# Performance work log

Hardware: AMD Instinct MI355X
Metric: run time of the kernel (lower is better)

## Reference

```python
import jax, jax.numpy as jnp
import numpy as np

HEADS = 4
REDUCTION = 4
BN_EPS = 1e-5


def conv1x1_bn(x, W, b, gamma, beta, mean, var):
    # x: [B, C, W, H]; 1x1 conv == channel matmul, then BN (inference form)
    y = jnp.einsum('oc,bcwh->bowh', W, x) + b[None, :, None, None]
    scale = (gamma / jnp.sqrt(var + BN_EPS))[None, :, None, None]
    return (y - mean[None, :, None, None]) * scale + beta[None, :, None, None]


def setup_inputs() -> dict:
    key = jax.random.key(0)
    ks = jax.random.split(key, 24)
    C, Cq = 512, 512 // REDUCTION  # 128
    B, Wd, Hd = 16, 32, 32
    dh = Cq // HEADS  # 32
    rnd = lambda k, s: jax.random.normal(k, s, dtype=jnp.float32)
    pos = lambda k, s: jax.random.uniform(k, s, dtype=jnp.float32, minval=0.5, maxval=1.5)
    return {
        'x': rnd(ks[0], (B, C, Wd, Hd)),
        'Wq': rnd(ks[1], (Cq, C)) * 0.05, 'bq': rnd(ks[2], (Cq,)) * 0.05,
        'q_gamma': pos(ks[3], (Cq,)), 'q_beta': rnd(ks[4], (Cq,)) * 0.05,
        'q_mean': rnd(ks[5], (Cq,)) * 0.05, 'q_var': pos(ks[6], (Cq,)),
        'Wk': rnd(ks[7], (Cq, C)) * 0.05, 'bk': rnd(ks[8], (Cq,)) * 0.05,
        'k_gamma': pos(ks[9], (Cq,)), 'k_beta': rnd(ks[10], (Cq,)) * 0.05,
        'k_mean': rnd(ks[11], (Cq,)) * 0.05, 'k_var': pos(ks[12], (Cq,)),
        'Wv': rnd(ks[13], (C, C)) * 0.05, 'bv': rnd(ks[14], (C,)) * 0.05,
        'v_gamma': pos(ks[15], (C,)), 'v_beta': rnd(ks[16], (C,)) * 0.05,
        'v_mean': rnd(ks[17], (C,)) * 0.05, 'v_var': pos(ks[18], (C,)),
        'rel_h': rnd(ks[19], (1, HEADS, dh, 1, Hd)),
        'rel_w': rnd(ks[20], (1, HEADS, dh, Wd, 1)),
    }


def reference(x, Wq, bq, q_gamma, q_beta, q_mean, q_var,
              Wk, bk, k_gamma, k_beta, k_mean, k_var,
              Wv, bv, v_gamma, v_beta, v_mean, v_var,
              rel_h, rel_w):
    B, C, Wd, Hd = x.shape
    N = Wd * Hd
    dh = C // REDUCTION // HEADS
    dv = C // HEADS
    q = conv1x1_bn(x, Wq, bq, q_gamma, q_beta, q_mean, q_var).reshape(B, HEADS, dh, N)
    k = conv1x1_bn(x, Wk, bk, k_gamma, k_beta, k_mean, k_var).reshape(B, HEADS, dh, N)
    v = conv1x1_bn(x, Wv, bv, v_gamma, v_beta, v_mean, v_var).reshape(B, HEADS, dv, N)
    # content-content: q^T k -> [B, H, N, N]
    cc = jnp.einsum('bhdn,bhdm->bhnm', q, k)
    # content-position: (rel_h + rel_w) flattened to [H, dh, N], then pos^T @ q
    pos = (rel_h + rel_w).reshape(HEADS, dh, N)
    cp = jnp.einsum('hdn,bhdm->bhnm', pos, q)
    attn = jax.nn.softmax(cc + cp, axis=-1)
    # out = v @ attn^T  (torch: matmul(v, attention.permute(0,1,3,2)))
    out = jnp.einsum('bhcn,bhmn->bhcm', v, attn)
    return out.reshape(B, C, Wd, Hd) + x
```

## Files before the change

kernel.cpp:

```cpp
#include <hip/hip_runtime.h>


typedef _Float16 f16x8 __attribute__((ext_vector_type(8)));
typedef __attribute__((ext_vector_type(4))) float f32x4;
typedef __attribute__((ext_vector_type(4))) unsigned int u32x4;
typedef __attribute__((ext_vector_type(2))) unsigned int u32x2;

#define MFMAH(a, b, c) __builtin_amdgcn_mfma_f32_16x16x32_f16(a, b, c, 0, 0, 0)
#define LOG2E 1.4426950408889634f

__device__ __forceinline__ unsigned pkh(float a, float b) {
  auto p = __builtin_amdgcn_cvt_pkrtz(a, b);
  return __builtin_bit_cast(unsigned, p);
}
__device__ __forceinline__ short f2h(float a) {
  _Float16 h = (_Float16)a;
  return __builtin_bit_cast(short, h);
}

__device__ __forceinline__ void gload16(const void* g, void* l) {
  __builtin_amdgcn_global_load_lds(
      (const __attribute__((address_space(1))) void*)g,
      (__attribute__((address_space(3))) void*)l, 16, 0, 0);
}

__global__ __launch_bounds__(256) void fold_kernel(
    const float* __restrict__ Wq, const float* __restrict__ bq,
    const float* __restrict__ qg, const float* __restrict__ qbe,
    const float* __restrict__ qme, const float* __restrict__ qva,
    const float* __restrict__ Wk, const float* __restrict__ bk,
    const float* __restrict__ kg, const float* __restrict__ kbe,
    const float* __restrict__ kme, const float* __restrict__ kva,
    const float* __restrict__ Wv, const float* __restrict__ bv,
    const float* __restrict__ vg, const float* __restrict__ vbe,
    const float* __restrict__ vme, const float* __restrict__ vva,
    unsigned short* __restrict__ Wh, float* __restrict__ bfv)
{
  int idx = blockIdx.x * 256 + threadIdx.x;
  if (idx >= 768 * 512) return;
  int o = idx >> 9, c = idx & 511;
  float w, sc, bb, mean, beta, post;
  if (o < 128) {
    sc = qg[o] / sqrtf(qva[o] + 1e-5f);
    w = Wq[o * 512 + c]; bb = bq[o]; mean = qme[o]; beta = qbe[o];
    post = LOG2E;
  } else if (o < 256) {
    int r = o - 128;
    sc = kg[r] / sqrtf(kva[r] + 1e-5f);
    w = Wk[r * 512 + c]; bb = bk[r]; mean = kme[r]; beta = kbe[r];
    post = 1.0f;
  } else {
    int r = o - 256;
    sc = vg[r] / sqrtf(vva[r] + 1e-5f);
    w = Wv[r * 512 + c]; bb = bv[r]; mean = vme[r]; beta = vbe[r];
    post = 1.0f;
  }
  Wh[idx] = (unsigned short)f2h(w * sc * post);
  if (c == 0) bfv[o] = ((bb - mean) * sc + beta) * post;
}

__global__ __launch_bounds__(256) void pos_kernel(
    const float* __restrict__ rel_h, const float* __restrict__ rel_w,
    unsigned short* __restrict__ posH)
{
  int idx = blockIdx.x * 256 + threadIdx.x;
  if (idx >= 4 * 1024 * 32) return;
  int h = idx >> 15, rem = idx & 32767, n = rem >> 5, d = rem & 31;
  int w = n >> 5, hh = n & 31;
  float v = rel_h[(h * 32 + d) * 32 + hh] + rel_w[(h * 32 + d) * 32 + w];
  posH[idx] = (unsigned short)f2h(v);
}

__global__ __launch_bounds__(256) void proj_kernel(
    const float* __restrict__ x,
    const unsigned short* __restrict__ Wh, const float* __restrict__ bfv,
    unsigned short* __restrict__ qH, unsigned short* __restrict__ kH,
    unsigned short* __restrict__ vH)
{
  __shared__ __align__(16) short sm[16384];
  short* At = sm;
  short* Bt = sm + 8192;

  int bid = blockIdx.x;
  int b = bid / 48, rem = bid % 48, mblk = rem >> 3, nblk = rem & 7;
  int Mb = mblk * 128, Nb = nblk * 128;
  int t = threadIdx.x;
  int lane = t & 63, wvid = t >> 6, ln = lane & 15, g = lane >> 4;
  int wm = wvid >> 1, wn = wvid & 1;
  int kgp = t >> 5, lp = t & 31;

  f32x4 acc[4][4];
  for (int i = 0; i < 4; i++)
    for (int j = 0; j < 4; j++) acc[i][j] = (f32x4){0.f, 0.f, 0.f, 0.f};

  for (int kb = 0; kb < 512; kb += 64) {
    __syncthreads();
    for (int ii = 0; ii < 4; ii++) {
      int idx = ii * 256 + t;
      int row = idx >> 3, pos = idx & 7;
      int j = pos ^ (row & 7);
      *(f16x8*)&At[row * 64 + pos * 8] =
          *(const f16x8*)&Wh[(Mb + row) * 512 + kb + j * 8];
    }
    for (int e = 0; e < 2; e++) {
      float2 f[8];
      for (int rr = 0; rr < 8; rr++)
        f[rr] = *(const float2*)&x[(b * 512 + kb + kgp * 8 + rr) * 1024 +
                                   Nb + 2 * lp + 64 * e];
      int n0 = 2 * lp + 64 * e, n1 = n0 + 1;
      u32x4 h0, h1;
      for (int pr = 0; pr < 4; pr++) {
        h0[pr] = pkh(f[2 * pr].x, f[2 * pr + 1].x);
        h1[pr] = pkh(f[2 * pr].y, f[2 * pr + 1].y);
      }
      *(u32x4*)&Bt[n0 * 64 + 8 * (kgp ^ (n0 & 7))] = h0;
      *(u32x4*)&Bt[n1 * 64 + 8 * (kgp ^ (n1 & 7))] = h1;
    }
    __syncthreads();

    f16x8 af[4][2], bf[4][2];
    for (int mt = 0; mt < 4; mt++)
      for (int ks = 0; ks < 2; ks++) {
        int o = wm * 64 + mt * 16 + ln;
        af[mt][ks] = *(const f16x8*)&At[o * 64 + 8 * ((ks * 4 + g) ^ (o & 7))];
      }
    for (int nt = 0; nt < 4; nt++)
      for (int ks = 0; ks < 2; ks++) {
        int n = wn * 64 + nt * 16 + ln;
        bf[nt][ks] = *(const f16x8*)&Bt[n * 64 + 8 * ((ks * 4 + g) ^ (n & 7))];
      }
    for (int ks = 0; ks < 2; ks++)
      for (int mt = 0; mt < 4; mt++)
        for (int nt = 0; nt < 4; nt++)
          acc[mt][nt] = MFMAH(af[mt][ks], bf[nt][ks], acc[mt][nt]);
  }

  unsigned* smU = (unsigned*)sm;
  for (int p = 0; p < 2; p++) {
    __syncthreads();
    if (wn == p) {
      if (mblk < 2) {
        for (int mt = 0; mt < 4; mt++)
          for (int nt = 0; nt < 4; nt++) {
            float y0 = acc[mt][nt][0] + bfv[Mb + wm * 64 + mt * 16 + g * 4 + 0];
            float y1 = acc[mt][nt][1] + bfv[Mb + wm * 64 + mt * 16 + g * 4 + 1];
            float y2 = acc[mt][nt][2] + bfv[Mb + wm * 64 + mt * 16 + g * 4 + 2];
            float y3 = acc[mt][nt][3] + bfv[Mb + wm * 64 + mt * 16 + g * 4 + 3];
            u32x2 pk = (u32x2){pkh(y0, y1), pkh(y2, y3)};
            int nl = nt * 16 + ln;
            *(u32x2*)&smU[nl * 66 + wm * 32 + mt * 8 + g * 2] = pk;
          }
      } else {
        for (int mt = 0; mt < 4; mt++)
          for (int nt = 0; nt < 4; nt++)
            for (int r = 0; r < 4; r++) {
              int o = wm * 64 + mt * 16 + g * 4 + r;
              sm[o * 72 + nt * 16 + ln] = f2h(acc[mt][nt][r] + bfv[Mb + o]);
            }
      }
    }
    __syncthreads();
    if (mblk < 2) {
      unsigned short* dh = (mblk == 0) ? qH : kH;
      for (int it = 0; it < 4; it++) {
        int task = it * 256 + t;
        int h = task >> 8, nl = (task >> 2) & 63, qc = task & 3;
        u32x4 v4 = *(const u32x4*)&smU[nl * 66 + h * 16 + qc * 4];
        int gi = ((b * 4 + h) * 1024 + Nb + p * 64 + nl) * 32 + qc * 8;
        *(u32x4*)&dh[gi] = v4;
      }
    } else {
      int bh = b * 4 + (mblk - 2);
      for (int it = 0; it < 4; it++) {
        int task = it * 256 + t;
        int o = task >> 3, qc = task & 7;
        u32x4 vv = *(const u32x4*)&sm[o * 72 + qc * 8];
        *(u32x4*)&vH[(bh * 128 + o) * 1024 + Nb + p * 64 + qc * 8] = vv;
      }
    }
  }
}

__global__ __launch_bounds__(512, 4) void attn_kernel(
    const float* __restrict__ x,
    const unsigned short* __restrict__ qH, const unsigned short* __restrict__ kH,
    const unsigned short* __restrict__ posH, const unsigned short* __restrict__ vH,
    float* __restrict__ out)
{
  __shared__ __align__(16) short sm[2 * 12288 + 8 * 1152];

  int bid = blockIdx.x;
  int bh = (bid & 7) * 8 + ((bid >> 3) & 7);
  int qt = bid >> 6;
  int b = bh >> 2, h = bh & 3;
  int t = threadIdx.x;
  int lane = t & 63, w = t >> 6, ln = lane & 15, g = (lane >> 4) & 3;

  int qrow = qt * 128 + w * 16 + ln;
  f16x8 bQ   = *(const f16x8*)&qH[(bh * 1024 + qrow) * 32 + g * 8];
  f16x8 bPos = *(const f16x8*)&posH[(h * 1024 + qrow) * 32 + g * 8];

  f16x8 aOnes;
  {
    _Float16 o1 = (ln == 0) ? (_Float16)1.0f : (_Float16)0.0f;
    for (int i = 0; i < 8; i++) aOnes[i] = o1;
  }

  f32x4 acc[9];
  for (int ct = 0; ct < 9; ct++) acc[ct] = (f32x4){0.f, 0.f, 0.f, 0.f};
  float m_run = -1e30f;

  short* Pw = &sm[24576 + w * 1152];

  auto STAGE = [&](int bb, int jb) {
    {
      int u = t & 255;
      int r = u >> 2;
      int ch = (u & 3) ^ (r & 3) ^ ((r >> 2) & 3);
      long gq = (long)(bh * 1024 + jb + r) * 32 + ch * 8;
      const unsigned short* src = (t < 256) ? kH : qH;
      short* base = &sm[bb * 12288 + ((t < 256) ? 0 : 2048) + (w & 3) * 512];
      gload16(&src[gq], base);
    }
    for (int i = 0; i < 2; i++) {
      int u = t + i * 512;
      int c = u >> 3;
      int vch = (u & 7) ^ (c & 7);
      long gv = (long)(bh * 128 + c) * 1024 + jb + vch * 8;
      short* base = &sm[bb * 12288 + 4096 + (w + i * 8) * 512];
      gload16(&vH[gv], base);
    }
  };

  STAGE(0, 0);

  for (int it = 0; it < 16; ++it) {
    int cur = it & 1;
    if (it < 15) {
      STAGE(cur ^ 1, (it + 1) * 64);
      asm volatile("s_waitcnt vmcnt(3)" ::: "memory");
    } else {
      asm volatile("s_waitcnt vmcnt(0)" ::: "memory");
    }
    __builtin_amdgcn_s_barrier();
    __builtin_amdgcn_sched_barrier(0);

    const short* B = &sm[cur * 12288];

    f16x8 aK[4], aQ[4];
    for (int kt = 0; kt < 4; kt++) {
      int r = kt * 16 + ln;
      int p = g ^ (r & 3) ^ ((r >> 2) & 3);
      int off = r * 32 + p * 8;
      aK[kt] = *(const f16x8*)&B[off];
      aQ[kt] = *(const f16x8*)&B[2048 + off];
    }

    f32x4 s[4];
    for (int kt = 0; kt < 4; kt++) s[kt] = (f32x4){0.f, 0.f, 0.f, 0.f};
    __builtin_amdgcn_s_setprio(1);
    for (int kt = 0; kt < 4; kt++) s[kt] = MFMAH(aK[kt], bQ, s[kt]);
    for (int kt = 0; kt < 4; kt++) s[kt] = MFMAH(aQ[kt], bPos, s[kt]);
    __builtin_amdgcn_s_setprio(0);

    float m0 = fmaxf(fmaxf(s[0][0], s[0][1]), fmaxf(s[0][2], s[0][3]));
    float m1 = fmaxf(fmaxf(s[1][0], s[1][1]), fmaxf(s[1][2], s[1][3]));
    float m2 = fmaxf(fmaxf(s[2][0], s[2][1]), fmaxf(s[2][2], s[2][3]));
    float m3 = fmaxf(fmaxf(s[3][0], s[3][1]), fmaxf(s[3][2], s[3][3]));
    float mx = fmaxf(fmaxf(m0, m1), fmaxf(m2, m3));
    if (__any(mx > m_run + 8.f)) {
      float mxf = fmaxf(mx, __shfl_xor(mx, 16));
      mxf = fmaxf(mxf, __shfl_xor(mxf, 32));
      float mnew = fmaxf(m_run, mxf);
      float scl = __builtin_amdgcn_exp2f(m_run - mnew);
      for (int ct = 0; ct < 9; ct++) acc[ct] *= scl;
      m_run = mnew;
    }
    for (int kt = 0; kt < 4; kt++)
      for (int r = 0; r < 4; r++)
        s[kt][r] = __builtin_amdgcn_exp2f(s[kt][r] - m_run);

    for (int kt = 0; kt < 4; kt++) {
      u32x2 pk = (u32x2){pkh(s[kt][0], s[kt][1]), pkh(s[kt][2], s[kt][3])};
      *(u32x2*)&Pw[ln * 72 + kt * 16 + g * 4] = pk;
    }
    asm volatile("s_waitcnt lgkmcnt(0)" ::: "memory");
    __builtin_amdgcn_sched_barrier(0);
    f16x8 pFrag[2];
    for (int st2 = 0; st2 < 2; st2++)
      pFrag[st2] = *(const f16x8*)&Pw[ln * 72 + st2 * 32 + g * 8];

    __builtin_amdgcn_s_setprio(1);
    for (int ct = 0; ct < 8; ct++)
      for (int st2 = 0; st2 < 2; st2++) {
        int c = ct * 16 + ln;
        int pos = (st2 * 4 + g) ^ (c & 7);
        f16x8 av = *(const f16x8*)&B[4096 + c * 64 + pos * 8];
        acc[ct] = MFMAH(av, pFrag[st2], acc[ct]);
      }
    acc[8] = MFMAH(aOnes, pFrag[0], acc[8]);
    acc[8] = MFMAH(aOnes, pFrag[1], acc[8]);
    __builtin_amdgcn_s_setprio(0);

    __builtin_amdgcn_sched_barrier(0);
    __builtin_amdgcn_s_barrier();
    __builtin_amdgcn_sched_barrier(0);
  }

  float lsum = __shfl(acc[8][0], ln);
  float inv = 1.0f / lsum;
  int m = qt * 128 + w * 16 + ln;
  for (int ct = 0; ct < 8; ct++)
    for (int r = 0; r < 4; r++) {
      int c = h * 128 + ct * 16 + g * 4 + r;
      int gi = (b * 512 + c) * 1024 + m;
      out[gi] = acc[ct][r] * inv + x[gi];
    }
}

extern "C" void kernel_launch(void* const* d_in, const int* in_sizes, int n_in,
                              void* d_out, int out_size, void* d_ws, size_t ws_size,
                              hipStream_t stream) {
  const float* x    = (const float*)d_in[0];
  const float* Wq   = (const float*)d_in[1];
  const float* bq   = (const float*)d_in[2];
  const float* qg   = (const float*)d_in[3];
  const float* qbe  = (const float*)d_in[4];
  const float* qme  = (const float*)d_in[5];
  const float* qva  = (const float*)d_in[6];
  const float* Wk   = (const float*)d_in[7];
  const float* bk   = (const float*)d_in[8];
  const float* kg   = (const float*)d_in[9];
  const float* kbe  = (const float*)d_in[10];
  const float* kme  = (const float*)d_in[11];
  const float* kva  = (const float*)d_in[12];
  const float* Wv   = (const float*)d_in[13];
  const float* bv   = (const float*)d_in[14];
  const float* vg   = (const float*)d_in[15];
  const float* vbe  = (const float*)d_in[16];
  const float* vme  = (const float*)d_in[17];
  const float* vva  = (const float*)d_in[18];
  const float* relh = (const float*)d_in[19];
  const float* relw = (const float*)d_in[20];
  float* outp = (float*)d_out;

  unsigned char* ws = (unsigned char*)d_ws;
  unsigned short* Whp  = (unsigned short*)(ws + 0);
  float*          bfv  = (float*)(ws + 786432);
  unsigned short* qHp  = (unsigned short*)(ws + 789504);
  unsigned short* kHp  = (unsigned short*)(ws + 4983808);
  unsigned short* posHp= (unsigned short*)(ws + 9178112);
  unsigned short* vHp  = (unsigned short*)(ws + 9440256);

  fold_kernel<<<1536, 256, 0, stream>>>(Wq, bq, qg, qbe, qme, qva,
                                        Wk, bk, kg, kbe, kme, kva,
                                        Wv, bv, vg, vbe, vme, vva,
                                        Whp, bfv);
  pos_kernel<<<512, 256, 0, stream>>>(relh, relw, posHp);
  proj_kernel<<<768, 256, 0, stream>>>(x, Whp, bfv, qHp, kHp, vHp);
  attn_kernel<<<512, 512, 0, stream>>>(x, qHp, kHp, posHp, vHp, outp);
}
```

Before: 87.59 us.

## Double-buffer projection GEMM with async weight loads and register-prefetched x tiles

Restructures the projection GEMM main loop into a double-buffered software pipeline over 32-wide K steps. Weight tiles are fetched straight into LDS with global_load_lds, and the x tile for the next step is held in registers and written to LDS after the current MFMAs. This overlaps global loads with compute and removes one barrier per iteration. In exchange it uses a smaller K step (16 iterations instead of 8), a new XOR swizzle, and an s_setprio boost around the MFMAs. The extra register pressure may cost occupancy.

```diff
diff --git a/kernel.cpp b/kernel.cpp
--- a/kernel.cpp
+++ b/kernel.cpp
@@ -17,6 +17,7 @@
   _Float16 h = (_Float16)a;
   return __builtin_bit_cast(short, h);
 }
+__device__ __forceinline__ int sfn(int x) { return (x & 3) ^ ((x >> 2) & 3); }
 
 __device__ __forceinline__ void gload16(const void* g, void* l) {
   __builtin_amdgcn_global_load_lds(
@@ -78,66 +79,85 @@
     unsigned short* __restrict__ vH)
 {
   __shared__ __align__(16) short sm[16384];
-  short* At = sm;
-  short* Bt = sm + 8192;
 
   int bid = blockIdx.x;
   int b = bid / 48, rem = bid % 48, mblk = rem >> 3, nblk = rem & 7;
   int Mb = mblk * 128, Nb = nblk * 128;
   int t = threadIdx.x;
-  int lane = t & 63, wvid = t >> 6, ln = lane & 15, g = lane >> 4;
-  int wm = wvid >> 1, wn = wvid & 1;
+  int lane = t & 63, w4 = t >> 6, ln = lane & 15, g = lane >> 4;
+  int wm = w4 >> 1, wn = w4 & 1;
   int kgp = t >> 5, lp = t & 31;
+  int n0b = 2 * lp, hh = kgp & 1, cch = kgp >> 1;
 
   f32x4 acc[4][4];
   for (int i = 0; i < 4; i++)
     for (int j = 0; j < 4; j++) acc[i][j] = (f32x4){0.f, 0.f, 0.f, 0.f};
 
-  for (int kb = 0; kb < 512; kb += 64) {
+  float2 fB[8];
+
+  auto ISSUE_B = [&](int kb) {
+    for (int e = 0; e < 2; e++)
+      for (int rr = 0; rr < 4; rr++)
+        fB[e * 4 + rr] = *(const float2*)&x[(b * 512 + kb + kgp * 4 + rr) * 1024 +
+                                            Nb + n0b + e * 64];
+  };
+  auto ISSUE_A = [&](int kb, int bb) {
+    for (int i = 0; i < 2; i++) {
+      int grp = w4 + i * 4;
+      int unit = grp * 64 + lane;
+      int row = unit >> 2, pos = unit & 3;
+      int j = pos ^ sfn(row);
+      gload16(&Wh[(Mb + row) * 512 + kb + j * 8], &sm[bb * 4096 + grp * 512]);
+    }
+  };
+  auto WRITE_B = [&](int bb) {
+    short* Bt = &sm[8192 + bb * 4096];
+    for (int e = 0; e < 2; e++) {
+      int n0 = n0b + e * 64, n1 = n0 + 1;
+      u32x2 w0 = (u32x2){pkh(fB[e * 4 + 0].x, fB[e * 4 + 1].x),
+                         pkh(fB[e * 4 + 2].x, fB[e * 4 + 3].x)};
+      u32x2 w1 = (u32x2){pkh(fB[e * 4 + 0].y, fB[e * 4 + 1].y),
+                         pkh(fB[e * 4 + 2].y, fB[e * 4 + 3].y)};
+      *(u32x2*)&Bt[n0 * 32 + (cch ^ sfn(n0)) * 8 + hh * 4] = w0;
+      *(u32x2*)&Bt[n1 * 32 + (cch ^ sfn(n1)) * 8 + hh * 4] = w1;
+    }
+  };
+
+  ISSUE_B(0);
+  ISSUE_A(0, 0);
+  WRITE_B(0);
+  __syncthreads();
+
+  for (int ik = 0; ik < 16; ++ik) {
+    int cur = ik & 1, nxt = cur ^ 1;
+    if (ik < 15) {
+      ISSUE_B((ik + 1) * 32);
+      ISSUE_A((ik + 1) * 32, nxt);
+    }
+    const short* Ac = &sm[cur * 4096];
+    const short* Bc = &sm[8192 + cur * 4096];
+    f16x8 af[4], bf[4];
+    for (int mt = 0; mt < 4; mt++) {
+      int o = wm * 64 + mt * 16 + ln;
+      af[mt] = *(const f16x8*)&Ac[o * 32 + (g ^ sfn(o)) * 8];
+    }
+    for (int nt = 0; nt < 4; nt++) {
+      int n = wn * 64 + nt * 16 + ln;
+      bf[nt] = *(const f16x8*)&Bc[n * 32 + (g ^ sfn(n)) * 8];
+    }
+    __builtin_amdgcn_s_setprio(1);
+    for (int mt = 0; mt < 4; mt++)
+      for (int nt = 0; nt < 4; nt++)
+        acc[mt][nt] = MFMAH(af[mt], bf[nt], acc[mt][nt]);
+    __builtin_amdgcn_s_setprio(0);
+    __builtin_amdgcn_sched_barrier(0);
+    if (ik < 15) WRITE_B(nxt);
     __syncthreads();
-    for (int ii = 0; ii < 4; ii++) {
-      int idx = ii * 256 + t;
-      int row = idx >> 3, pos = idx & 7;
-      int j = pos ^ (row & 7);
-      *(f16x8*)&At[row * 64 + pos * 8] =
-          *(const f16x8*)&Wh[(Mb + row) * 512 + kb + j * 8];
-    }
-    for (int e = 0; e < 2; e++) {
-      float2 f[8];
-      for (int rr = 0; rr < 8; rr++)
-        f[rr] = *(const float2*)&x[(b * 512 + kb + kgp * 8 + rr) * 1024 +
-                                   Nb + 2 * lp + 64 * e];
-      int n0 = 2 * lp + 64 * e, n1 = n0 + 1;
-      u32x4 h0, h1;
-      for (int pr = 0; pr < 4; pr++) {
-        h0[pr] = pkh(f[2 * pr].x, f[2 * pr + 1].x);
-        h1[pr] = pkh(f[2 * pr].y, f[2 * pr + 1].y);
-      }
-      *(u32x4*)&Bt[n0 * 64 + 8 * (kgp ^ (n0 & 7))] = h0;
-      *(u32x4*)&Bt[n1 * 64 + 8 * (kgp ^ (n1 & 7))] = h1;
-    }
-    __syncthreads();
-
-    f16x8 af[4][2], bf[4][2];
-    for (int mt = 0; mt < 4; mt++)
-      for (int ks = 0; ks < 2; ks++) {
-        int o = wm * 64 + mt * 16 + ln;
-        af[mt][ks] = *(const f16x8*)&At[o * 64 + 8 * ((ks * 4 + g) ^ (o & 7))];
-      }
-    for (int nt = 0; nt < 4; nt++)
-      for (int ks = 0; ks < 2; ks++) {
-        int n = wn * 64 + nt * 16 + ln;
-        bf[nt][ks] = *(const f16x8*)&Bt[n * 64 + 8 * ((ks * 4 + g) ^ (n & 7))];
-      }
-    for (int ks = 0; ks < 2; ks++)
-      for (int mt = 0; mt < 4; mt++)
-        for (int nt = 0; nt < 4; nt++)
-          acc[mt][nt] = MFMAH(af[mt][ks], bf[nt][ks], acc[mt][nt]);
   }
 
   unsigned* smU = (unsigned*)sm;
   for (int p = 0; p < 2; p++) {
-    __syncthreads();
+    if (p) __syncthreads();
     if (wn == p) {
       if (mblk < 2) {
         for (int mt = 0; mt < 4; mt++)
```

New measurement: 87.80 us. Within noise of the previous version (+0.2%).

## Widen projection tile to 128x256 with 512 threads and async weight loads

Applied to the files above, without the earlier changes.

The projection GEMM kernel now uses 512-thread blocks, each computing a 128x256 output tile, which halves the grid and reuses each weight tile across twice as many columns. Weight tiles go straight to LDS through global_load_lds. The x tile is converted to fp16 with swizzled stores whose order alternates to spread LDS bank traffic, and the MFMA section is wrapped in s_setprio. The larger tile cuts redundant weight traffic but leaves fewer blocks (384) to fill the GPU's compute units and raises LDS use per block.

```diff
diff --git a/kernel.cpp b/kernel.cpp
--- a/kernel.cpp
+++ b/kernel.cpp
@@ -71,23 +71,23 @@
   posH[idx] = (unsigned short)f2h(v);
 }
 
-__global__ __launch_bounds__(256) void proj_kernel(
+__global__ __launch_bounds__(512) void proj_kernel(
     const float* __restrict__ x,
     const unsigned short* __restrict__ Wh, const float* __restrict__ bfv,
     unsigned short* __restrict__ qH, unsigned short* __restrict__ kH,
     unsigned short* __restrict__ vH)
 {
-  __shared__ __align__(16) short sm[16384];
-  short* At = sm;
-  short* Bt = sm + 8192;
+  __shared__ __align__(16) short sm[24576];
 
   int bid = blockIdx.x;
-  int b = bid / 48, rem = bid % 48, mblk = rem >> 3, nblk = rem & 7;
-  int Mb = mblk * 128, Nb = nblk * 128;
+  int b = bid / 24, rem = bid % 24, mblk = rem >> 2, nblk = rem & 3;
+  int Mb = mblk * 128, Nb = nblk * 256;
   int t = threadIdx.x;
-  int lane = t & 63, wvid = t >> 6, ln = lane & 15, g = lane >> 4;
-  int wm = wvid >> 1, wn = wvid & 1;
-  int kgp = t >> 5, lp = t & 31;
+  int lane = t & 63, w = t >> 6, ln = lane & 15, g = (lane >> 4) & 3;
+  int wm = w >> 2, wn = w & 3;
+  int kg = t >> 7, np = t & 127;
+  int n0 = 2 * np;
+  int swp = (np >> 2) & 1;
 
   f32x4 acc[4][4];
   for (int i = 0; i < 4; i++)
@@ -95,48 +95,60 @@
 
   for (int kb = 0; kb < 512; kb += 64) {
     __syncthreads();
-    for (int ii = 0; ii < 4; ii++) {
-      int idx = ii * 256 + t;
-      int row = idx >> 3, pos = idx & 7;
+    for (int i = 0; i < 2; i++) {
+      int grp = w + i * 8;
+      int unit = grp * 64 + lane;
+      int row = unit >> 3, pos = unit & 7;
       int j = pos ^ (row & 7);
-      *(f16x8*)&At[row * 64 + pos * 8] =
-          *(const f16x8*)&Wh[(Mb + row) * 512 + kb + j * 8];
-    }
-    for (int e = 0; e < 2; e++) {
-      float2 f[8];
-      for (int rr = 0; rr < 8; rr++)
-        f[rr] = *(const float2*)&x[(b * 512 + kb + kgp * 8 + rr) * 1024 +
-                                   Nb + 2 * lp + 64 * e];
-      int n0 = 2 * lp + 64 * e, n1 = n0 + 1;
-      u32x4 h0, h1;
-      for (int pr = 0; pr < 4; pr++) {
-        h0[pr] = pkh(f[2 * pr].x, f[2 * pr + 1].x);
-        h1[pr] = pkh(f[2 * pr].y, f[2 * pr + 1].y);
-      }
-      *(u32x4*)&Bt[n0 * 64 + 8 * (kgp ^ (n0 & 7))] = h0;
-      *(u32x4*)&Bt[n1 * 64 + 8 * (kgp ^ (n1 & 7))] = h1;
+      gload16(&Wh[(Mb + row) * 512 + kb + j * 8], &sm[grp * 512]);
+    }
+    {
+      float2 fB[16];
+      for (int rr = 0; rr < 16; rr++)
+        fB[rr] = *(const float2*)&x[(b * 512 + kb + kg * 16 + rr) * 1024 +
+                                    Nb + n0];
+      short* Bt = sm + 8192;
+      for (int s = 0; s < 2; s++) {
+        u32x4 wE = (u32x4){pkh(fB[s * 8 + 0].x, fB[s * 8 + 1].x),
+                           pkh(fB[s * 8 + 2].x, fB[s * 8 + 3].x),
+                           pkh(fB[s * 8 + 4].x, fB[s * 8 + 5].x),
+                           pkh(fB[s * 8 + 6].x, fB[s * 8 + 7].x)};
+        u32x4 wO = (u32x4){pkh(fB[s * 8 + 0].y, fB[s * 8 + 1].y),
+                           pkh(fB[s * 8 + 2].y, fB[s * 8 + 3].y),
+                           pkh(fB[s * 8 + 4].y, fB[s * 8 + 5].y),
+                           pkh(fB[s * 8 + 6].y, fB[s * 8 + 7].y)};
+        int k8 = kg * 2 + s;
+        int offE = n0 * 64 + 8 * (k8 ^ (n0 & 7));
+        int offO = (n0 + 1) * 64 + 8 * (k8 ^ ((n0 + 1) & 7));
+        int o1 = swp ? offO : offE, o2 = swp ? offE : offO;
+        u32x4 d1 = swp ? wO : wE, d2 = swp ? wE : wO;
+        *(u32x4*)&Bt[o1] = d1;
+        *(u32x4*)&Bt[o2] = d2;
+      }
     }
     __syncthreads();
 
-    f16x8 af[4][2], bf[4][2];
-    for (int mt = 0; mt < 4; mt++)
-      for (int ks = 0; ks < 2; ks++) {
+    const short* Bt = sm + 8192;
+    for (int ks = 0; ks < 2; ks++) {
+      f16x8 af[4], bf[4];
+      for (int mt = 0; mt < 4; mt++) {
         int o = wm * 64 + mt * 16 + ln;
-        af[mt][ks] = *(const f16x8*)&At[o * 64 + 8 * ((ks * 4 + g) ^ (o & 7))];
-      }
-    for (int nt = 0; nt < 4; nt++)
-      for (int ks = 0; ks < 2; ks++) {
+        af[mt] = *(const f16x8*)&sm[o * 64 + 8 * ((ks * 4 + g) ^ (o & 7))];
+      }
+      for (int nt = 0; nt < 4; nt++) {
         int n = wn * 64 + nt * 16 + ln;
-        bf[nt][ks] = *(const f16x8*)&Bt[n * 64 + 8 * ((ks * 4 + g) ^ (n & 7))];
-      }
-    for (int ks = 0; ks < 2; ks++)
+        bf[nt] = *(const f16x8*)&Bt[n * 64 + 8 * ((ks * 4 + g) ^ (n & 7))];
+      }
+      __builtin_amdgcn_s_setprio(1);
       for (int mt = 0; mt < 4; mt++)
         for (int nt = 0; nt < 4; nt++)
-          acc[mt][nt] = MFMAH(af[mt][ks], bf[nt][ks], acc[mt][nt]);
+          acc[mt][nt] = MFMAH(af[mt], bf[nt], acc[mt][nt]);
+      __builtin_amdgcn_s_setprio(0);
+    }
   }
 
   unsigned* smU = (unsigned*)sm;
-  for (int p = 0; p < 2; p++) {
+  for (int p = 0; p < 4; p++) {
     __syncthreads();
     if (wn == p) {
       if (mblk < 2) {
@@ -162,8 +174,8 @@
     __syncthreads();
     if (mblk < 2) {
       unsigned short* dh = (mblk == 0) ? qH : kH;
-      for (int it = 0; it < 4; it++) {
-        int task = it * 256 + t;
+      for (int it = 0; it < 2; it++) {
+        int task = it * 512 + t;
         int h = task >> 8, nl = (task >> 2) & 63, qc = task & 3;
         u32x4 v4 = *(const u32x4*)&smU[nl * 66 + h * 16 + qc * 4];
         int gi = ((b * 4 + h) * 1024 + Nb + p * 64 + nl) * 32 + qc * 8;
@@ -171,8 +183,8 @@
       }
     } else {
       int bh = b * 4 + (mblk - 2);
-      for (int it = 0; it < 4; it++) {
-        int task = it * 256 + t;
+      for (int it = 0; it < 2; it++) {
+        int task = it * 512 + t;
         int o = task >> 3, qc = task & 7;
         u32x4 vv = *(const u32x4*)&sm[o * 72 + qc * 8];
         *(u32x4*)&vH[(bh * 128 + o) * 1024 + Nb + p * 64 + qc * 8] = vv;
@@ -357,6 +369,6 @@
                                         Wv, bv, vg, vbe, vme, vva,
                                         Whp, bfv);
   pos_kernel<<<512, 256, 0, stream>>>(relh, relw, posHp);
-  proj_kernel<<<768, 256, 0, stream>>>(x, Whp, bfv, qHp, kHp, vHp);
+  proj_kernel<<<384, 512, 0, stream>>>(x, Whp, bfv, qHp, kHp, vHp);
   attn_kernel<<<512, 512, 0, stream>>>(x, qHp, kHp, posHp, vHp, outp);
 }
```

After: 84.37 us. 3.7% less time.
